# Kernel optimization log

Hardware: AMD Instinct MI355X
Metric: run time of the kernel (lower is better)

Reference implementation:

```python
import jax, jax.numpy as jnp
import numpy as np

B, S, H, E, V, P = 64, 1024, 512, 512, 32000, 40


def setup_inputs() -> dict:
    key = jax.random.key(0)
    ks = jax.random.split(key, 18)
    s = 0.05  # weight scale to keep tanh/sigmoid in active range
    inp = {}
    inp["input_token"] = jax.random.randint(ks[0], (B,), 0, V, dtype=jnp.int32)
    inp["hidden"] = jax.random.normal(ks[1], (1, B, H), jnp.float32)
    inp["cell"] = jax.random.normal(ks[2], (1, B, H), jnp.float32)
    inp["encoder_outputs"] = jax.random.normal(ks[3], (B, S, H), jnp.float32)
    pos_ids = jax.random.randint(ks[4], (B, S), 0, P)
    inp["pos_onehot"] = jax.nn.one_hot(pos_ids, P, dtype=jnp.float32)
    inp["src_mask"] = jnp.zeros((B, S), dtype=bool)  # no PAD (avoids all -inf rows)
    # learned parameters (torch Linear convention: y = x @ W.T + b)
    inp["embed_table"] = jax.random.normal(ks[5], (V, E), jnp.float32) * s
    inp["W_s"] = jax.random.normal(ks[6], (H, H), jnp.float32) * s
    inp["W_h"] = jax.random.normal(ks[7], (H, H), jnp.float32) * s
    inp["V_w"] = jax.random.normal(ks[8], (H,), jnp.float32) * s
    inp["W_p"] = jax.random.normal(ks[9], (P,), jnp.float32) * s
    inp["b_p"] = jax.random.normal(ks[10], (), jnp.float32) * s
    inp["W_ih"] = jax.random.normal(ks[11], (4 * H, E + H), jnp.float32) * s
    inp["W_hh"] = jax.random.normal(ks[12], (4 * H, H), jnp.float32) * s
    inp["b_ih"] = jax.random.normal(ks[13], (4 * H,), jnp.float32) * s
    inp["b_hh"] = jax.random.normal(ks[14], (4 * H,), jnp.float32) * s
    inp["W_out"] = jax.random.normal(ks[15], (V, H), jnp.float32) * s
    inp["b_out"] = jax.random.normal(ks[16], (V,), jnp.float32) * s
    return inp


def reference(input_token, hidden, cell, encoder_outputs, pos_onehot, src_mask,
              embed_table, W_s, W_h, V_w, W_p, b_p,
              W_ih, W_hh, b_ih, b_hh, W_out, b_out):
    # embedding (dropout is identity in eval)
    emb = embed_table[input_token]                                  # (B, E)
    q = hidden[-1]                                                  # (B, H)
    # POS-gated Bahdanau attention
    qs = q @ W_s.T                                                  # (B, H)
    eh = jnp.einsum('bsh,kh->bsk', encoder_outputs, W_h)            # (B, S, H)
    energy = jnp.tanh(qs[:, None, :] + eh)                          # (B, S, H)
    scores = jnp.einsum('bsh,h->bs', energy, V_w)                   # (B, S)
    gate = jax.nn.sigmoid(pos_onehot @ W_p + b_p)                   # (B, S)
    gated = jnp.where(src_mask, jnp.float32(-1e30), scores * gate)
    attn = jax.nn.softmax(gated, axis=-1)                           # (B, S)
    context = jnp.einsum('bs,bsh->bh', attn, encoder_outputs)       # (B, H)
    # single-step, single-layer LSTM (torch gate order: i, f, g, o)
    lstm_in = jnp.concatenate([emb, context], axis=-1)              # (B, E+H)
    gates = lstm_in @ W_ih.T + hidden[0] @ W_hh.T + b_ih + b_hh     # (B, 4H)
    i, f, g, o = jnp.split(gates, 4, axis=-1)
    c1 = jax.nn.sigmoid(f) * cell[0] + jax.nn.sigmoid(i) * jnp.tanh(g)
    h1 = jax.nn.sigmoid(o) * jnp.tanh(c1)                           # (B, H)
    pred = h1 @ W_out.T + b_out                                     # (B, V)
    return (pred, h1[None], c1[None], attn)
```

## Files before the change

kernel.cpp:

```cpp
#include <hip/hip_runtime.h>

#define BB 64
#define SS 1024
#define HH 512
#define EE 512
#define VV 32000
#define PP 40

typedef __attribute__((ext_vector_type(8))) __bf16 bf16x8;
typedef __attribute__((ext_vector_type(4))) float f32x4;
typedef __attribute__((ext_vector_type(8))) unsigned short us8_t;
typedef __attribute__((ext_vector_type(4))) unsigned short us4_t;

__device__ inline float fast_tanh(float x) {
    float e = __expf(-2.0f * fabsf(x));
    float t = (1.0f - e) / (1.0f + e);
    return copysignf(t, x);
}
__device__ inline float sigmf(float x) { return 1.0f / (1.0f + __expf(-x)); }

__device__ inline unsigned int cvtpk(float lo, float hi) {
    unsigned int r;
    asm volatile("v_cvt_pk_bf16_f32 %0, %1, %2" : "=v"(r) : "v"(lo), "v"(hi));
    return r;
}
__device__ inline us8_t pack8c(float4 x, float4 y) {
    union { unsigned int u[4]; us8_t v; } r;
    r.u[0] = cvtpk(x.x, x.y); r.u[1] = cvtpk(x.z, x.w);
    r.u[2] = cvtpk(y.x, y.y); r.u[3] = cvtpk(y.z, y.w);
    return r.v;
}

#define LST 36

__global__ __launch_bounds__(256)
void k_prep(const float* __restrict__ hidden, const float* __restrict__ Ws,
            const float* __restrict__ Wh, const float* __restrict__ pos,
            const float* __restrict__ Wp, const float* __restrict__ bp,
            unsigned short* __restrict__ wh16, float* __restrict__ qs,
            float* __restrict__ gate, float* __restrict__ ctx) {
    int blk = blockIdx.x, t = threadIdx.x;
    if (blk < 64) {
        __shared__ float hb[HH];
        int b = blk;
        for (int i = t; i < HH; i += 256) hb[i] = hidden[b * HH + i];
        __syncthreads();
        for (int n = t; n < HH; n += 256) {
            const float* wr = Ws + (size_t)n * HH;
            float acc = 0.0f;
#pragma unroll 4
            for (int k = 0; k < HH; k += 4) {
                float4 w = *(const float4*)(wr + k);
                acc += w.x * hb[k] + w.y * hb[k + 1] + w.z * hb[k + 2] + w.w * hb[k + 3];
            }
            qs[b * HH + n] = acc;
        }
    } else if (blk < 96) {
        int base = (blk - 64) * 8192 + t * 4;
#pragma unroll
        for (int j = 0; j < 8; ++j) {
            int idx = base + j * 1024;
            float4 x = *(const float4*)(Wh + idx);
            union { unsigned int u[2]; us4_t v; } r;
            r.u[0] = cvtpk(x.x, x.y); r.u[1] = cvtpk(x.z, x.w);
            *(us4_t*)(wh16 + idx) = r.v;
        }
    } else if (blk < 352) {
        int idx = (blk - 96) * 256 + t;
        const float* pr = pos + (size_t)idx * PP;
        float acc = bp[0];
#pragma unroll
        for (int j = 0; j < 10; ++j) {
            float4 x = *(const float4*)(pr + j * 4);
            acc += x.x * Wp[j * 4] + x.y * Wp[j * 4 + 1] + x.z * Wp[j * 4 + 2] + x.w * Wp[j * 4 + 3];
        }
        gate[idx] = sigmf(acc);
    } else {
        int idx = (blk - 352) * 256 + t;
#pragma unroll
        for (int j = 0; j < 16; ++j) ctx[idx * 16 + j] = 0.0f;
    }
}

__global__ __launch_bounds__(256)
void k_scores(const float* __restrict__ enc, const unsigned short* __restrict__ wh16,
              const float* __restrict__ qs, const float* __restrict__ Vw,
              float* __restrict__ part) {
    __shared__ unsigned short As[128 * LST];
    __shared__ unsigned short Bs[128 * LST];
    __shared__ float pbuf[2][128];
    int bid = blockIdx.x;
    int nh = bid >> 9, rest = bid & 511;
    int b = rest >> 3, sc = rest & 7;
    int s0 = sc * 128, n0 = nh * 128;
    int tid = threadIdx.x;
    int w = tid >> 6, lane = tid & 63;
    int wm = w >> 1, wn = w & 1;
    int l15 = lane & 15, lq = lane >> 4;

    float qv[4], vw[4];
#pragma unroll
    for (int nf = 0; nf < 4; ++nf) {
        int n = n0 + wn * 64 + nf * 16 + l15;
        qv[nf] = qs[b * HH + n];
        vw[nf] = Vw[n];
    }

    int ar = tid >> 1, half = tid & 1;
    const float* aSrc = enc + ((size_t)(b * SS + s0 + ar)) * HH + half * 16;
    const unsigned short* bSrc = wh16 + (size_t)(n0 + ar) * HH + half * 16;
    int aOff = ar * LST + half * 16;
    int bOff = ar * LST + half * 16;

    int aRd[4], bRd[4];
#pragma unroll
    for (int mf = 0; mf < 4; ++mf) aRd[mf] = (wm * 64 + mf * 16 + l15) * LST + lq * 8;
#pragma unroll
    for (int nf = 0; nf < 4; ++nf) bRd[nf] = (wn * 64 + nf * 16 + l15) * LST + lq * 8;

    f32x4 acc[4][4];
#pragma unroll
    for (int mf = 0; mf < 4; ++mf)
#pragma unroll
        for (int nf = 0; nf < 4; ++nf) acc[mf][nf] = (f32x4){0.f, 0.f, 0.f, 0.f};

    {
        float4 a0 = *(const float4*)(aSrc);
        float4 a1 = *(const float4*)(aSrc + 4);
        float4 a2 = *(const float4*)(aSrc + 8);
        float4 a3 = *(const float4*)(aSrc + 12);
        us8_t b0 = *(const us8_t*)(bSrc);
        us8_t b1 = *(const us8_t*)(bSrc + 8);
        *(us8_t*)(As + aOff) = pack8c(a0, a1);
        *(us8_t*)(As + aOff + 8) = pack8c(a2, a3);
        *(us8_t*)(Bs + bOff) = b0;
        *(us8_t*)(Bs + bOff + 8) = b1;
    }
    float4 xa0 = *(const float4*)(aSrc + 32);
    float4 xa1 = *(const float4*)(aSrc + 36);
    float4 xa2 = *(const float4*)(aSrc + 40);
    float4 xa3 = *(const float4*)(aSrc + 44);
    us8_t xb0 = *(const us8_t*)(bSrc + 32);
    us8_t xb1 = *(const us8_t*)(bSrc + 40);
    asm volatile("s_waitcnt lgkmcnt(0)" ::: "memory");
    __builtin_amdgcn_s_barrier();

#pragma unroll
    for (int st = 0; st < 16; ++st) {
        float4 ya0, ya1, ya2, ya3; us8_t yb0, yb1;
        if (st < 14) {
            const float* ga = aSrc + (st + 2) * 32;
            ya0 = *(const float4*)(ga);
            ya1 = *(const float4*)(ga + 4);
            ya2 = *(const float4*)(ga + 8);
            ya3 = *(const float4*)(ga + 12);
            const unsigned short* gb = bSrc + (st + 2) * 32;
            yb0 = *(const us8_t*)(gb);
            yb1 = *(const us8_t*)(gb + 8);
        }
        us8_t af[4], bf[4];
#pragma unroll
        for (int mf = 0; mf < 4; ++mf) af[mf] = *(const us8_t*)(As + aRd[mf]);
#pragma unroll
        for (int nf = 0; nf < 4; ++nf) bf[nf] = *(const us8_t*)(Bs + bRd[nf]);
        asm volatile("s_waitcnt lgkmcnt(0)" ::: "memory");
        __builtin_amdgcn_s_barrier();
        if (st < 15) {
            *(us8_t*)(As + aOff) = pack8c(xa0, xa1);
            *(us8_t*)(As + aOff + 8) = pack8c(xa2, xa3);
            *(us8_t*)(Bs + bOff) = xb0;
            *(us8_t*)(Bs + bOff + 8) = xb1;
        }
#pragma unroll
        for (int mf = 0; mf < 4; ++mf)
#pragma unroll
            for (int nf = 0; nf < 4; ++nf)
                acc[mf][nf] = __builtin_amdgcn_mfma_f32_16x16x32_bf16(
                    __builtin_bit_cast(bf16x8, af[mf]),
                    __builtin_bit_cast(bf16x8, bf[nf]), acc[mf][nf], 0, 0, 0);
        asm volatile("s_waitcnt lgkmcnt(0)" ::: "memory");
        __builtin_amdgcn_s_barrier();
        if (st < 14) { xa0 = ya0; xa1 = ya1; xa2 = ya2; xa3 = ya3; xb0 = yb0; xb1 = yb1; }
    }

#pragma unroll
    for (int mf = 0; mf < 4; ++mf)
#pragma unroll
        for (int r = 0; r < 4; ++r) {
            float p = 0.0f;
#pragma unroll
            for (int nf = 0; nf < 4; ++nf)
                p += vw[nf] * fast_tanh(acc[mf][nf][r] + qv[nf]);
            p += __shfl_xor(p, 1, 64);
            p += __shfl_xor(p, 2, 64);
            p += __shfl_xor(p, 4, 64);
            p += __shfl_xor(p, 8, 64);
            if (l15 == 0) pbuf[wn][wm * 64 + mf * 16 + lq * 4 + r] = p;
        }
    __syncthreads();
    if (tid < 128) {
        part[nh * (BB * SS) + b * SS + s0 + tid] = pbuf[0][tid] + pbuf[1][tid];
    }
}

__global__ __launch_bounds__(256)
void k_context(const float* __restrict__ enc, const float* __restrict__ part,
               const float* __restrict__ gate, const unsigned char* __restrict__ mask,
               float* __restrict__ attn, float* __restrict__ ctx) {
    int b = blockIdx.x >> 4, chunk = blockIdx.x & 15;
    int s0 = chunk * 64, t = threadIdx.x;
    int w = t >> 6, ln = t & 63;
    float sum = 0.0f;
#pragma unroll
    for (int j = 0; j < 4; ++j) {
        int s = j * 256 + t;
        float raw = part[b * SS + s] + part[BB * SS + b * SS + s]
                  + part[2 * BB * SS + b * SS + s] + part[3 * BB * SS + b * SS + s];
        float v = mask[b * SS + s] ? -1e30f : raw * gate[b * SS + s];
        sum += __expf(v);
    }
#pragma unroll
    for (int off = 1; off < 64; off <<= 1) sum += __shfl_xor(sum, off, 64);
    __shared__ float sl[4];
    if (ln == 0) sl[w] = sum;
    __syncthreads();
    float inv = 1.0f / (sl[0] + sl[1] + sl[2] + sl[3]);

    __shared__ float aw[64];
    if (t < 64) {
        int s = s0 + t;
        float raw = part[b * SS + s] + part[BB * SS + b * SS + s]
                  + part[2 * BB * SS + b * SS + s] + part[3 * BB * SS + b * SS + s];
        float v = mask[b * SS + s] ? -1e30f : raw * gate[b * SS + s];
        float a = __expf(v) * inv;
        aw[t] = a;
        attn[b * SS + s] = a;
    }
    __syncthreads();

    const float* eb = enc + ((size_t)(b * SS + s0)) * HH + 2 * t;
    float a0 = 0.f, a1 = 0.f;
#pragma unroll 4
    for (int s = 0; s < 64; ++s) {
        float2 u = *(const float2*)(eb + (size_t)s * HH);
        a0 += aw[s] * u.x;
        a1 += aw[s] * u.y;
    }
    atomicAdd(&ctx[b * HH + 2 * t], a0);
    atomicAdd(&ctx[b * HH + 2 * t + 1], a1);
}

__global__ __launch_bounds__(256)
void k_build(const int* __restrict__ tok, const float* __restrict__ embt,
             const float* __restrict__ ctx, const float* __restrict__ hidden,
             unsigned short* __restrict__ li16, unsigned short* __restrict__ h16v) {
    int b = blockIdx.x, t = threadIdx.x;
    const float* er = embt + (size_t)tok[b] * EE;
    for (int i = 2 * t; i < HH; i += 512) {
        *(unsigned int*)(li16 + b * 1024 + i) = cvtpk(er[i], er[i + 1]);
        *(unsigned int*)(li16 + b * 1024 + 512 + i) = cvtpk(ctx[b * HH + i], ctx[b * HH + i + 1]);
        *(unsigned int*)(h16v + b * HH + i) = cvtpk(hidden[b * HH + i], hidden[b * HH + i + 1]);
    }
}

__global__ __launch_bounds__(256)
void k_gates(const unsigned short* __restrict__ li16, const unsigned short* __restrict__ h16v,
             const float* __restrict__ Wih, const float* __restrict__ Whh,
             float* __restrict__ gpart) {
    int nt = blockIdx.x >> 2, ksl = blockIdx.x & 3;
    int wave = threadIdx.x >> 6, lane = threadIdx.x & 63;
    int l15 = lane & 15, lq = lane >> 4, k0 = lq * 8;
    int n0w = nt * 128 + wave * 32;
    f32x4 acc[4][2];
#pragma unroll
    for (int mf = 0; mf < 4; ++mf)
#pragma unroll
        for (int nf = 0; nf < 2; ++nf) acc[mf][nf] = (f32x4){0.f, 0.f, 0.f, 0.f};

    for (int ks = 0; ks < 12; ++ks) {
        int kg = ksl * 384 + ks * 32;
        us8_t af[4];
        if (kg < 1024) {
#pragma unroll
            for (int mf = 0; mf < 4; ++mf)
                af[mf] = *(const us8_t*)(li16 + (mf * 16 + l15) * 1024 + kg + k0);
        } else {
#pragma unroll
            for (int mf = 0; mf < 4; ++mf)
                af[mf] = *(const us8_t*)(h16v + (mf * 16 + l15) * 512 + (kg - 1024) + k0);
        }
#pragma unroll
        for (int nf = 0; nf < 2; ++nf) {
            int n = n0w + nf * 16 + l15;
            us8_t bu;
            if (kg < 1024) {
                const float* wr = Wih + (size_t)n * 1024 + kg + k0;
                bu = pack8c(*(const float4*)wr, *(const float4*)(wr + 4));
            } else {
                const float* wr = Whh + (size_t)n * 512 + (kg - 1024) + k0;
                bu = pack8c(*(const float4*)wr, *(const float4*)(wr + 4));
            }
#pragma unroll
            for (int mf = 0; mf < 4; ++mf)
                acc[mf][nf] = __builtin_amdgcn_mfma_f32_16x16x32_bf16(
                    __builtin_bit_cast(bf16x8, af[mf]),
                    __builtin_bit_cast(bf16x8, bu), acc[mf][nf], 0, 0, 0);
        }
    }
#pragma unroll
    for (int mf = 0; mf < 4; ++mf)
#pragma unroll
        for (int nf = 0; nf < 2; ++nf)
#pragma unroll
            for (int r = 0; r < 4; ++r) {
                int row = mf * 16 + lq * 4 + r;
                int n = n0w + nf * 16 + l15;
                gpart[ksl * (BB * 2048) + row * 2048 + n] = acc[mf][nf][r];
            }
}

__global__ __launch_bounds__(512)
void k_lstm(const float* __restrict__ gpart, const float* __restrict__ bih,
            const float* __restrict__ bhh, const float* __restrict__ cell,
            float* __restrict__ oh, float* __restrict__ oc,
            unsigned short* __restrict__ h116) {
    int b = blockIdx.x, t = threadIdx.x;
    float gi = bih[t] + bhh[t];
    float gf = bih[512 + t] + bhh[512 + t];
    float gg = bih[1024 + t] + bhh[1024 + t];
    float go = bih[1536 + t] + bhh[1536 + t];
#pragma unroll
    for (int ksl = 0; ksl < 4; ++ksl) {
        const float* gp = gpart + ksl * (BB * 2048) + b * 2048;
        gi += gp[t];
        gf += gp[512 + t];
        gg += gp[1024 + t];
        go += gp[1536 + t];
    }
    float c0 = cell[b * HH + t];
    float c1 = sigmf(gf) * c0 + sigmf(gi) * fast_tanh(gg);
    float h1 = sigmf(go) * fast_tanh(c1);
    oh[b * HH + t] = h1;
    oc[b * HH + t] = c1;
    h116[b * HH + t] = (unsigned short)(cvtpk(h1, h1) & 0xffffu);
}

__global__ __launch_bounds__(512)
void k_pred(const unsigned short* __restrict__ h116, const float* __restrict__ Wout,
            const float* __restrict__ bout, float* __restrict__ pred) {
    int wave = threadIdx.x >> 6, lane = threadIdx.x & 63;
    int l15 = lane & 15, lq = lane >> 4, k0 = lq * 8;
    int n = blockIdx.x * 128 + wave * 16 + l15;
    f32x4 acc[4];
#pragma unroll
    for (int mf = 0; mf < 4; ++mf) acc[mf] = (f32x4){0.f, 0.f, 0.f, 0.f};
    const float* wr = Wout + (size_t)n * HH;
#pragma unroll 4
    for (int ks = 0; ks < 16; ++ks) {
        float4 x = *(const float4*)(wr + ks * 32 + k0);
        float4 y = *(const float4*)(wr + ks * 32 + k0 + 4);
        us8_t bu = pack8c(x, y);
#pragma unroll
        for (int mf = 0; mf < 4; ++mf) {
            us8_t au = *(const us8_t*)(h116 + (mf * 16 + l15) * 512 + ks * 32 + k0);
            acc[mf] = __builtin_amdgcn_mfma_f32_16x16x32_bf16(
                __builtin_bit_cast(bf16x8, au),
                __builtin_bit_cast(bf16x8, bu), acc[mf], 0, 0, 0);
        }
    }
    float bo = bout[n];
#pragma unroll
    for (int mf = 0; mf < 4; ++mf)
#pragma unroll
        for (int r = 0; r < 4; ++r) {
            int row = mf * 16 + lq * 4 + r;
            pred[(size_t)row * VV + n] = acc[mf][r] + bo;
        }
}

extern "C" void kernel_launch(void* const* d_in, const int* in_sizes, int n_in,
                              void* d_out, int out_size, void* d_ws, size_t ws_size,
                              hipStream_t stream) {
    const int* tok = (const int*)d_in[0];
    const float* hidden = (const float*)d_in[1];
    const float* cell = (const float*)d_in[2];
    const float* enc = (const float*)d_in[3];
    const float* pos = (const float*)d_in[4];
    const unsigned char* mask = (const unsigned char*)d_in[5];
    const float* embt = (const float*)d_in[6];
    const float* Ws = (const float*)d_in[7];
    const float* Wh = (const float*)d_in[8];
    const float* Vw = (const float*)d_in[9];
    const float* Wp = (const float*)d_in[10];
    const float* bp = (const float*)d_in[11];
    const float* Wih = (const float*)d_in[12];
    const float* Whh = (const float*)d_in[13];
    const float* bih = (const float*)d_in[14];
    const float* bhh = (const float*)d_in[15];
    const float* Wout = (const float*)d_in[16];
    const float* bout = (const float*)d_in[17];

    float* out = (float*)d_out;
    float* pred = out;
    float* out_h = out + 2048000;
    float* out_c = out + 2080768;
    float* attn = out + 2113536;

    char* wsb = (char*)d_ws;
    unsigned short* wh16 = (unsigned short*)(wsb);
    float* qs = (float*)(wsb + (512 << 10));
    float* gate = (float*)(wsb + (640 << 10));
    float* part = (float*)(wsb + (896 << 10));
    float* ctx = (float*)(wsb + (1920 << 10));
    unsigned short* li16 = (unsigned short*)(wsb + (2048 << 10));
    unsigned short* h16v = (unsigned short*)(wsb + (2176 << 10));
    float* gpart = (float*)(wsb + (2240 << 10));
    unsigned short* h116 = (unsigned short*)(wsb + (4288 << 10));

    hipLaunchKernelGGL(k_prep, dim3(360), dim3(256), 0, stream,
                       hidden, Ws, Wh, pos, Wp, bp, wh16, qs, gate, ctx);
    hipLaunchKernelGGL(k_scores, dim3(2048), dim3(256), 0, stream,
                       enc, wh16, qs, Vw, part);
    hipLaunchKernelGGL(k_context, dim3(1024), dim3(256), 0, stream,
                       enc, part, gate, mask, attn, ctx);
    hipLaunchKernelGGL(k_build, dim3(64), dim3(256), 0, stream,
                       tok, embt, ctx, hidden, li16, h16v);
    hipLaunchKernelGGL(k_gates, dim3(64), dim3(256), 0, stream, li16, h16v, Wih, Whh, gpart);
    hipLaunchKernelGGL(k_lstm, dim3(64), dim3(512), 0, stream,
                       gpart, bih, bhh, cell, out_h, out_c, h116);
    hipLaunchKernelGGL(k_pred, dim3(250), dim3(512), 0, stream, h116, Wout, bout, pred);
}
```

Baseline: 185.8 us.

## Pre-convert encoder outputs to bf16 and stage score tiles via direct LDS loads

The prep kernel gains a pass that converts the full encoder output tensor to bf16 in workspace. The scores kernel then loads bf16 A and B tiles straight into double-buffered, XOR-swizzled LDS with global_load_lds, replacing the per-thread register staging and fp32-to-bf16 packing. The context kernel also reads the bf16 copy. The goal is to cut repeated fp32 encoder traffic, since each of the four N-slices used to reread it in fp32. In exchange it adds a full conversion pass, a large workspace buffer that overlaps later scratch regions, and lower precision in the context sum.

```diff
diff --git a/kernel.cpp b/kernel.cpp
--- a/kernel.cpp
+++ b/kernel.cpp
@@ -31,14 +31,20 @@
     return r.v;
 }
 
-#define LST 36
+typedef __attribute__((address_space(1))) const unsigned char gas_t;
+typedef __attribute__((address_space(3))) unsigned char las_t;
+__device__ inline void gload16(const void* g, void* l) {
+    __builtin_amdgcn_global_load_lds((gas_t*)g, (las_t*)l, 16, 0, 0);
+}
 
 __global__ __launch_bounds__(256)
 void k_prep(const float* __restrict__ hidden, const float* __restrict__ Ws,
             const float* __restrict__ Wh, const float* __restrict__ pos,
             const float* __restrict__ Wp, const float* __restrict__ bp,
+            const float* __restrict__ enc,
             unsigned short* __restrict__ wh16, float* __restrict__ qs,
-            float* __restrict__ gate, float* __restrict__ ctx) {
+            float* __restrict__ gate, float* __restrict__ ctx,
+            unsigned short* __restrict__ enc16) {
     int blk = blockIdx.x, t = threadIdx.x;
     if (blk < 64) {
         __shared__ float hb[HH];
@@ -75,19 +81,30 @@
             acc += x.x * Wp[j * 4] + x.y * Wp[j * 4 + 1] + x.z * Wp[j * 4 + 2] + x.w * Wp[j * 4 + 3];
         }
         gate[idx] = sigmf(acc);
+    } else if (blk < 360) {
+        int idx = (blk - 352) * 256 + t;
+#pragma unroll
+        for (int j = 0; j < 16; ++j) ctx[idx * 16 + j] = 0.0f;
     } else {
-        int idx = (blk - 352) * 256 + t;
-#pragma unroll
-        for (int j = 0; j < 16; ++j) ctx[idx * 16 + j] = 0.0f;
+        size_t base = (size_t)(blk - 360) * 16384 + (size_t)t * 4;
+#pragma unroll
+        for (int j = 0; j < 16; ++j) {
+            size_t idx = base + (size_t)j * 1024;
+            float4 x = *(const float4*)(enc + idx);
+            union { unsigned int u[2]; us4_t v; } r;
+            r.u[0] = cvtpk(x.x, x.y); r.u[1] = cvtpk(x.z, x.w);
+            *(us4_t*)(enc16 + idx) = r.v;
+        }
     }
 }
 
 __global__ __launch_bounds__(256)
-void k_scores(const float* __restrict__ enc, const unsigned short* __restrict__ wh16,
+void k_scores(const unsigned short* __restrict__ enc16,
+              const unsigned short* __restrict__ wh16,
               const float* __restrict__ qs, const float* __restrict__ Vw,
               float* __restrict__ part) {
-    __shared__ unsigned short As[128 * LST];
-    __shared__ unsigned short Bs[128 * LST];
+    __shared__ unsigned short As[2][8192];
+    __shared__ unsigned short Bs[2][8192];
     __shared__ float pbuf[2][128];
     int bid = blockIdx.x;
     int nh = bid >> 9, rest = bid & 511;
@@ -106,17 +123,17 @@
         vw[nf] = Vw[n];
     }
 
-    int ar = tid >> 1, half = tid & 1;
-    const float* aSrc = enc + ((size_t)(b * SS + s0 + ar)) * HH + half * 16;
-    const unsigned short* bSrc = wh16 + (size_t)(n0 + ar) * HH + half * 16;
-    int aOff = ar * LST + half * 16;
-    int bOff = ar * LST + half * 16;
-
-    int aRd[4], bRd[4];
-#pragma unroll
-    for (int mf = 0; mf < 4; ++mf) aRd[mf] = (wm * 64 + mf * 16 + l15) * LST + lq * 8;
-#pragma unroll
-    for (int nf = 0; nf < 4; ++nf) bRd[nf] = (wn * 64 + nf * 16 + l15) * LST + lq * 8;
+    unsigned int colb = (unsigned int)(((lane & 7) * 16) ^ ((lane >> 3) << 4));
+    const char* gA0 = (const char*)(enc16 + (size_t)(b * SS + s0) * HH);
+    const char* gB0 = (const char*)(wh16 + (size_t)n0 * HH);
+    int rbase = w * 32 + (lane >> 3);
+
+    int aswz = (l15 & 7) << 4;
+    int aRowB[4], bRowB[4];
+#pragma unroll
+    for (int mf = 0; mf < 4; ++mf) aRowB[mf] = (wm * 64 + mf * 16 + l15) * 128;
+#pragma unroll
+    for (int nf = 0; nf < 4; ++nf) bRowB[nf] = (wn * 64 + nf * 16 + l15) * 128;
 
     f32x4 acc[4][4];
 #pragma unroll
@@ -124,64 +141,61 @@
 #pragma unroll
         for (int nf = 0; nf < 4; ++nf) acc[mf][nf] = (f32x4){0.f, 0.f, 0.f, 0.f};
 
-    {
-        float4 a0 = *(const float4*)(aSrc);
-        float4 a1 = *(const float4*)(aSrc + 4);
-        float4 a2 = *(const float4*)(aSrc + 8);
-        float4 a3 = *(const float4*)(aSrc + 12);
-        us8_t b0 = *(const us8_t*)(bSrc);
-        us8_t b1 = *(const us8_t*)(bSrc + 8);
-        *(us8_t*)(As + aOff) = pack8c(a0, a1);
-        *(us8_t*)(As + aOff + 8) = pack8c(a2, a3);
-        *(us8_t*)(Bs + bOff) = b0;
-        *(us8_t*)(Bs + bOff + 8) = b1;
-    }
-    float4 xa0 = *(const float4*)(aSrc + 32);
-    float4 xa1 = *(const float4*)(aSrc + 36);
-    float4 xa2 = *(const float4*)(aSrc + 40);
-    float4 xa3 = *(const float4*)(aSrc + 44);
-    us8_t xb0 = *(const us8_t*)(bSrc + 32);
-    us8_t xb1 = *(const us8_t*)(bSrc + 40);
-    asm volatile("s_waitcnt lgkmcnt(0)" ::: "memory");
+#define STAGE(BUF, KT)                                                          \
+    {                                                                           \
+        _Pragma("unroll")                                                       \
+        for (int i = 0; i < 4; ++i) {                                           \
+            int row = rbase + i * 8;                                            \
+            const char* ga = gA0 + (size_t)row * 1024 + (KT) * 128 + colb;      \
+            const char* gb = gB0 + (size_t)row * 1024 + (KT) * 128 + colb;      \
+            char* la = (char*)As[BUF] + (w * 32 + i * 8) * 128;                 \
+            char* lb = (char*)Bs[BUF] + (w * 32 + i * 8) * 128;                 \
+            gload16(ga, la);                                                    \
+            gload16(gb, lb);                                                    \
+        }                                                                       \
+    }
+
+#define COMPUTE(BUF)                                                            \
+    {                                                                           \
+        _Pragma("unroll")                                                       \
+        for (int ks = 0; ks < 2; ++ks) {                                        \
+            us8_t af[4], bf[4];                                                 \
+            _Pragma("unroll")                                                   \
+            for (int mf = 0; mf < 4; ++mf)                                      \
+                af[mf] = *(const us8_t*)((const char*)As[BUF] + aRowB[mf] +     \
+                                         ((ks * 64 + lq * 16) ^ aswz));         \
+            _Pragma("unroll")                                                   \
+            for (int nf = 0; nf < 4; ++nf)                                      \
+                bf[nf] = *(const us8_t*)((const char*)Bs[BUF] + bRowB[nf] +     \
+                                         ((ks * 64 + lq * 16) ^ aswz));         \
+            _Pragma("unroll")                                                   \
+            for (int mf = 0; mf < 4; ++mf)                                      \
+                _Pragma("unroll")                                               \
+                for (int nf = 0; nf < 4; ++nf)                                  \
+                    acc[mf][nf] = __builtin_amdgcn_mfma_f32_16x16x32_bf16(      \
+                        __builtin_bit_cast(bf16x8, af[mf]),                     \
+                        __builtin_bit_cast(bf16x8, bf[nf]), acc[mf][nf], 0, 0, 0); \
+        }                                                                       \
+    }
+
+    STAGE(0, 0);
+    asm volatile("s_waitcnt vmcnt(0)" ::: "memory");
     __builtin_amdgcn_s_barrier();
 
 #pragma unroll
-    for (int st = 0; st < 16; ++st) {
-        float4 ya0, ya1, ya2, ya3; us8_t yb0, yb1;
-        if (st < 14) {
-            const float* ga = aSrc + (st + 2) * 32;
-            ya0 = *(const float4*)(ga);
-            ya1 = *(const float4*)(ga + 4);
-            ya2 = *(const float4*)(ga + 8);
-            ya3 = *(const float4*)(ga + 12);
-            const unsigned short* gb = bSrc + (st + 2) * 32;
-            yb0 = *(const us8_t*)(gb);
-            yb1 = *(const us8_t*)(gb + 8);
-        }
-        us8_t af[4], bf[4];
-#pragma unroll
-        for (int mf = 0; mf < 4; ++mf) af[mf] = *(const us8_t*)(As + aRd[mf]);
-#pragma unroll
-        for (int nf = 0; nf < 4; ++nf) bf[nf] = *(const us8_t*)(Bs + bRd[nf]);
-        asm volatile("s_waitcnt lgkmcnt(0)" ::: "memory");
+    for (int kt2 = 0; kt2 < 4; ++kt2) {
+        int kt = kt2 * 2;
+        if (kt < 7) STAGE(1, kt + 1);
+        COMPUTE(0);
+        asm volatile("s_waitcnt vmcnt(0)" ::: "memory");
         __builtin_amdgcn_s_barrier();
-        if (st < 15) {
-            *(us8_t*)(As + aOff) = pack8c(xa0, xa1);
-            *(us8_t*)(As + aOff + 8) = pack8c(xa2, xa3);
-            *(us8_t*)(Bs + bOff) = xb0;
-            *(us8_t*)(Bs + bOff + 8) = xb1;
-        }
-#pragma unroll
-        for (int mf = 0; mf < 4; ++mf)
-#pragma unroll
-            for (int nf = 0; nf < 4; ++nf)
-                acc[mf][nf] = __builtin_amdgcn_mfma_f32_16x16x32_bf16(
-                    __builtin_bit_cast(bf16x8, af[mf]),
-                    __builtin_bit_cast(bf16x8, bf[nf]), acc[mf][nf], 0, 0, 0);
-        asm volatile("s_waitcnt lgkmcnt(0)" ::: "memory");
+        if (kt + 1 < 7) STAGE(0, kt + 2);
+        COMPUTE(1);
+        asm volatile("s_waitcnt vmcnt(0)" ::: "memory");
         __builtin_amdgcn_s_barrier();
-        if (st < 14) { xa0 = ya0; xa1 = ya1; xa2 = ya2; xa3 = ya3; xb0 = yb0; xb1 = yb1; }
-    }
+    }
+#undef STAGE
+#undef COMPUTE
 
 #pragma unroll
     for (int mf = 0; mf < 4; ++mf)
@@ -204,7 +218,7 @@
 }
 
 __global__ __launch_bounds__(256)
-void k_context(const float* __restrict__ enc, const float* __restrict__ part,
+void k_context(const unsigned short* __restrict__ enc16, const float* __restrict__ part,
                const float* __restrict__ gate, const unsigned char* __restrict__ mask,
                float* __restrict__ attn, float* __restrict__ ctx) {
     int b = blockIdx.x >> 4, chunk = blockIdx.x & 15;
@@ -238,13 +252,13 @@
     }
     __syncthreads();
 
-    const float* eb = enc + ((size_t)(b * SS + s0)) * HH + 2 * t;
+    const unsigned short* eb = enc16 + ((size_t)(b * SS + s0)) * HH + 2 * t;
     float a0 = 0.f, a1 = 0.f;
 #pragma unroll 4
     for (int s = 0; s < 64; ++s) {
-        float2 u = *(const float2*)(eb + (size_t)s * HH);
-        a0 += aw[s] * u.x;
-        a1 += aw[s] * u.y;
+        unsigned int u = *(const unsigned int*)(eb + (size_t)s * HH);
+        a0 += aw[s] * __uint_as_float(u << 16);
+        a1 += aw[s] * __uint_as_float(u & 0xffff0000u);
     }
     atomicAdd(&ctx[b * HH + 2 * t], a0);
     atomicAdd(&ctx[b * HH + 2 * t + 1], a1);
@@ -414,15 +428,16 @@
     float* ctx = (float*)(wsb + (1920 << 10));
     unsigned short* li16 = (unsigned short*)(wsb + (2048 << 10));
     unsigned short* h16v = (unsigned short*)(wsb + (2176 << 10));
+    unsigned short* enc16 = (unsigned short*)(wsb + (2240 << 10));
     float* gpart = (float*)(wsb + (2240 << 10));
     unsigned short* h116 = (unsigned short*)(wsb + (4288 << 10));
 
-    hipLaunchKernelGGL(k_prep, dim3(360), dim3(256), 0, stream,
-                       hidden, Ws, Wh, pos, Wp, bp, wh16, qs, gate, ctx);
+    hipLaunchKernelGGL(k_prep, dim3(2408), dim3(256), 0, stream,
+                       hidden, Ws, Wh, pos, Wp, bp, enc, wh16, qs, gate, ctx, enc16);
     hipLaunchKernelGGL(k_scores, dim3(2048), dim3(256), 0, stream,
-                       enc, wh16, qs, Vw, part);
+                       enc16, wh16, qs, Vw, part);
     hipLaunchKernelGGL(k_context, dim3(1024), dim3(256), 0, stream,
-                       enc, part, gate, mask, attn, ctx);
+                       enc16, part, gate, mask, attn, ctx);
     hipLaunchKernelGGL(k_build, dim3(64), dim3(256), 0, stream,
                        tok, embt, ctx, hidden, li16, h16v);
     hipLaunchKernelGGL(k_gates, dim3(64), dim3(256), 0, stream, li16, h16v, Wih, Whh, gpart);
```

New measurement: 199.0 us. +7.2%, slower.
